# Kernel tuning notes

Measured on AMD Instinct MI355X. Metric: run time of the kernel, lower is better.

The kernel has to match this reference:

```python
import jax, jax.numpy as jnp
import numpy as np
import math

B, T, C = 4, 1024, 768
H, K = 12, 10
D = C // H  # 64


def setup_inputs() -> dict:
    key = jax.random.key(0)
    ks = jax.random.split(key, 8)
    s = 1.0 / math.sqrt(C)
    return {
        "hidden_states": jax.random.normal(ks[0], (B, T, C), jnp.float32),
        "ucb_count_score": jax.random.uniform(ks[1], (B, H, T, T), jnp.float32),
        "Wq": jax.random.normal(ks[2], (C, C), jnp.float32) * s,
        "bq": jnp.zeros((C,), jnp.float32),
        "Wk": jax.random.normal(ks[3], (C, C), jnp.float32) * s,
        "bk": jnp.zeros((C,), jnp.float32),
        "Wv": jax.random.normal(ks[4], (C, C), jnp.float32) * s,
        "bv": jnp.zeros((C,), jnp.float32),
        "Wo": jax.random.normal(ks[5], (C, C), jnp.float32) * s,
        "bo": jnp.zeros((C,), jnp.float32),
        "counter": 2000,
        "ucb": 1,
    }


def _heads(x):
    # [B,T,C] -> [B,H,T,D]
    return x.reshape(B, T, H, D).transpose(0, 2, 1, 3)


def reference(hidden_states, ucb_count_score, Wq, bq, Wk, bk, Wv, bv, Wo, bo, counter, ucb):
    q = _heads(hidden_states @ Wq + bq)
    k = _heads(hidden_states @ Wk + bk)
    v = _heads(hidden_states @ Wv + bv)

    scores = jnp.einsum("bhqd,bhkd->bhqk", q, k) / math.sqrt(D)
    att = jax.nn.softmax(scores, axis=-1)

    if ucb and counter >= 1000:  # ucb_activation_step
        log_t = math.log(float(counter))
        ucb_scores = att + 1.0 * jnp.sqrt(log_t / (ucb_count_score + 1e-8))  # ucb_beta=1.0
        _, top_idx = jax.lax.top_k(ucb_scores, K)  # [B,H,T,K]
        # scatter 1.0 at top-k positions along last axis
        flat_idx = top_idx.reshape(-1, K)            # [N,K], N=B*H*T
        n = flat_idx.shape[0]
        mask = jnp.zeros((n, T), att.dtype).at[jnp.arange(n)[:, None], flat_idx].set(1.0)
        mask = mask.reshape(B, H, T, T)
        updated_count = ucb_count_score + mask
        sel = att * mask
        attention_probs = sel / (sel.sum(axis=-1, keepdims=True) + 1e-8)
    else:
        attention_probs = att
        updated_count = ucb_count_score

    ctx = jnp.einsum("bhqk,bhkd->bhqd", attention_probs, v)
    ctx = ctx.transpose(0, 2, 1, 3).reshape(B, T, C)
    out = ctx @ Wo + bo  # proj_dropout is identity in eval
    return out, attention_probs, updated_count
```

## Files before the change

### kernel.cpp

```cpp
#include <hip/hip_runtime.h>
#include <math.h>

namespace {

constexpr int Bc = 4, Tc = 1024, Cch = 768, Hc = 12, Dc = 64, KSEL = 10;
constexpr size_t BTC    = (size_t)Bc * Tc * Cch;
constexpr size_t PROBSN = (size_t)Bc * Hc * Tc * Tc;
constexpr size_t CC     = (size_t)Cch * Cch;

typedef __attribute__((ext_vector_type(8))) short          bf16x8;
typedef __attribute__((ext_vector_type(4))) float          f32x4;
typedef __attribute__((ext_vector_type(4))) unsigned short u16x4;
typedef __attribute__((ext_vector_type(8))) unsigned short u16x8;

__device__ __forceinline__ unsigned short bf16rne(float x) {
  unsigned int u = __float_as_uint(x);
  return (unsigned short)((u + 0x7FFFu + ((u >> 16) & 1u)) >> 16);
}
__device__ __forceinline__ float bf16tof(unsigned short h) {
  return __uint_as_float(((unsigned int)h) << 16);
}

__global__ __launch_bounds__(256) void split_plane(
    const float* __restrict__ src,
    unsigned short* __restrict__ h, unsigned short* __restrict__ l)
{
  const size_t i = (size_t)(blockIdx.x * 256 + threadIdx.x) * 4;
  const float4 v = *(const float4*)&src[i];
  const float xs[4] = {v.x, v.y, v.z, v.w};
  u16x4 hh, ll;
  #pragma unroll
  for (int e = 0; e < 4; ++e) {
    const unsigned short hb = bf16rne(xs[e]);
    hh[e] = hb;
    ll[e] = bf16rne(xs[e] - bf16tof(hb));
  }
  *(u16x4*)&h[i] = hh;
  *(u16x4*)&l[i] = ll;
}

__global__ __launch_bounds__(256) void splitT_w(
    const float* __restrict__ W,
    unsigned short* __restrict__ th, unsigned short* __restrict__ tl)
{
  __shared__ float tile[32][33];
  const int n0 = blockIdx.x * 32, k0 = blockIdx.y * 32;
  const int x = threadIdx.x & 31, y = threadIdx.x >> 5;

  #pragma unroll
  for (int i = 0; i < 4; ++i) {
    const int kk = y * 4 + i;
    tile[kk][x] = W[(size_t)(k0 + kk) * Cch + n0 + x];
  }
  __syncthreads();
  #pragma unroll
  for (int i = 0; i < 4; ++i) {
    const int nn = y * 4 + i;
    const float v = tile[x][nn];
    const unsigned short hb = bf16rne(v);
    th[(size_t)(n0 + nn) * Cch + k0 + x] = hb;
    tl[(size_t)(n0 + nn) * Cch + k0 + x] = bf16rne(v - bf16tof(hb));
  }
}

__global__ __launch_bounds__(256) void qkv_mfma(
    const unsigned short* __restrict__ hidh, const unsigned short* __restrict__ hidl,
    const unsigned short* __restrict__ wqth, const unsigned short* __restrict__ wqtl,
    const unsigned short* __restrict__ wkth, const unsigned short* __restrict__ wktl,
    const unsigned short* __restrict__ wvth, const unsigned short* __restrict__ wvtl,
    const float* __restrict__ bq, const float* __restrict__ bk,
    const float* __restrict__ bv,
    unsigned short* __restrict__ qh, unsigned short* __restrict__ ql,
    unsigned short* __restrict__ kh, unsigned short* __restrict__ kl,
    float* __restrict__ V)
{
  const int z = blockIdx.z;
  const unsigned short* __restrict__ Bhp = (z == 0) ? wqth : (z == 1) ? wkth : wvth;
  const unsigned short* __restrict__ Blp = (z == 0) ? wqtl : (z == 1) ? wktl : wvtl;
  const float* __restrict__ bias = (z == 0) ? bq : (z == 1) ? bk : bv;

  const int m0 = blockIdx.y * 64;
  const int n0 = blockIdx.x * 128;

  __shared__ unsigned short Ah[64][72],  Al[64][72];
  __shared__ unsigned short Bh[128][72], Bl[128][72];

  const int t    = threadIdx.x;
  const int lane = t & 63;
  const int wv   = t >> 6;
  const int wq   = (wv >> 1) * 32;
  const int wk   = (wv & 1) * 64;
  const int fr   = lane & 15;
  const int fg   = lane >> 4;

  f32x4 acc[2][4] = {};

  for (int k0 = 0; k0 < Cch; k0 += 64) {
    __syncthreads();
    #pragma unroll
    for (int i = 0; i < 2; ++i) {
      const int id = t + 256*i;
      const int r = id >> 3, c8 = (id & 7) * 8;
      *(u16x8*)&Ah[r][c8] = *(const u16x8*)&hidh[(size_t)(m0 + r)*Cch + k0 + c8];
      *(u16x8*)&Al[r][c8] = *(const u16x8*)&hidl[(size_t)(m0 + r)*Cch + k0 + c8];
    }
    #pragma unroll
    for (int i = 0; i < 4; ++i) {
      const int id = t + 256*i;
      const int r = id >> 3, c8 = (id & 7) * 8;
      *(u16x8*)&Bh[r][c8] = *(const u16x8*)&Bhp[(size_t)(n0 + r)*Cch + k0 + c8];
      *(u16x8*)&Bl[r][c8] = *(const u16x8*)&Blp[(size_t)(n0 + r)*Cch + k0 + c8];
    }
    __syncthreads();

    #pragma unroll
    for (int g2 = 0; g2 < 2; ++g2) {
      const int dof = g2*32 + 8*fg;
      bf16x8 aH[2], aL[2];
      #pragma unroll
      for (int qt = 0; qt < 2; ++qt) {
        aH[qt] = *(const bf16x8*)&Ah[wq + qt*16 + fr][dof];
        aL[qt] = *(const bf16x8*)&Al[wq + qt*16 + fr][dof];
      }
      #pragma unroll
      for (int kt = 0; kt < 4; ++kt) {
        const bf16x8 bH = *(const bf16x8*)&Bh[wk + kt*16 + fr][dof];
        const bf16x8 bL = *(const bf16x8*)&Bl[wk + kt*16 + fr][dof];
        #pragma unroll
        for (int qt = 0; qt < 2; ++qt) {
          acc[qt][kt] = __builtin_amdgcn_mfma_f32_16x16x32_bf16(
              aH[qt], bH, acc[qt][kt], 0, 0, 0);
          acc[qt][kt] = __builtin_amdgcn_mfma_f32_16x16x32_bf16(
              aH[qt], bL, acc[qt][kt], 0, 0, 0);
          acc[qt][kt] = __builtin_amdgcn_mfma_f32_16x16x32_bf16(
              aL[qt], bH, acc[qt][kt], 0, 0, 0);
        }
      }
    }
  }

  float bcol[4];
  #pragma unroll
  for (int kt = 0; kt < 4; ++kt) bcol[kt] = bias[n0 + wk + kt*16 + fr];

  unsigned short* __restrict__ dh = (z == 0) ? qh : kh;
  unsigned short* __restrict__ dl = (z == 0) ? ql : kl;

  #pragma unroll
  for (int qt = 0; qt < 2; ++qt) {
    #pragma unroll
    for (int j = 0; j < 4; ++j) {
      const int m  = m0 + wq + qt*16 + 4*fg + j;
      const int b  = m >> 10, tt = m & 1023;
      #pragma unroll
      for (int kt = 0; kt < 4; ++kt) {
        const int col = n0 + wk + kt*16 + fr;
        const float val = acc[qt][kt][j] + bcol[kt];
        const size_t idx =
            (((size_t)(b*Hc + (col >> 6)))*Tc + tt)*Dc + (col & 63);
        if (z < 2) {
          const unsigned short hb = bf16rne(val);
          dh[idx] = hb;
          dl[idx] = bf16rne(val - bf16tof(hb));
        } else {
          V[idx] = val;
        }
      }
    }
  }
}

__global__ __launch_bounds__(256) void score_mfma(
    const unsigned short* __restrict__ qhp, const unsigned short* __restrict__ qlp,
    const unsigned short* __restrict__ khp, const unsigned short* __restrict__ klp,
    float* __restrict__ scores)
{
  const int k0 = blockIdx.x * 128;
  const int q0 = blockIdx.y * 64;
  const int bh = blockIdx.z;

  __shared__ unsigned short Qh[64][72],  Ql[64][72];
  __shared__ unsigned short Kh[128][72], Kl[128][72];

  const int t = threadIdx.x;
  const size_t qb = ((size_t)bh*Tc + q0) * Dc;
  const size_t kb = ((size_t)bh*Tc + k0) * Dc;

  #pragma unroll
  for (int i = 0; i < 2; ++i) {
    const int id = t + 256*i;
    const int r = id >> 3, c8 = (id & 7) * 8;
    *(u16x8*)&Qh[r][c8] = *(const u16x8*)&qhp[qb + (size_t)r*Dc + c8];
    *(u16x8*)&Ql[r][c8] = *(const u16x8*)&qlp[qb + (size_t)r*Dc + c8];
  }
  #pragma unroll
  for (int i = 0; i < 4; ++i) {
    const int id = t + 256*i;
    const int r = id >> 3, c8 = (id & 7) * 8;
    *(u16x8*)&Kh[r][c8] = *(const u16x8*)&khp[kb + (size_t)r*Dc + c8];
    *(u16x8*)&Kl[r][c8] = *(const u16x8*)&klp[kb + (size_t)r*Dc + c8];
  }
  __syncthreads();

  const int lane = t & 63;
  const int wv   = t >> 6;
  const int wq   = (wv >> 1) * 32;
  const int wk   = (wv & 1) * 64;
  const int fr   = lane & 15;
  const int fg   = lane >> 4;

  f32x4 acc[2][4] = {};

  #pragma unroll
  for (int g2 = 0; g2 < 2; ++g2) {
    const int dof = g2*32 + 8*fg;
    bf16x8 aH[2], aL[2];
    #pragma unroll
    for (int qt = 0; qt < 2; ++qt) {
      aH[qt] = *(const bf16x8*)&Qh[wq + qt*16 + fr][dof];
      aL[qt] = *(const bf16x8*)&Ql[wq + qt*16 + fr][dof];
    }
    #pragma unroll
    for (int kt = 0; kt < 4; ++kt) {
      const bf16x8 bH = *(const bf16x8*)&Kh[wk + kt*16 + fr][dof];
      const bf16x8 bL = *(const bf16x8*)&Kl[wk + kt*16 + fr][dof];
      #pragma unroll
      for (int qt = 0; qt < 2; ++qt) {
        acc[qt][kt] = __builtin_amdgcn_mfma_f32_16x16x32_bf16(
            aH[qt], bH, acc[qt][kt], 0, 0, 0);
        acc[qt][kt] = __builtin_amdgcn_mfma_f32_16x16x32_bf16(
            aH[qt], bL, acc[qt][kt], 0, 0, 0);
        acc[qt][kt] = __builtin_amdgcn_mfma_f32_16x16x32_bf16(
            aL[qt], bH, acc[qt][kt], 0, 0, 0);
      }
    }
  }

  #pragma unroll
  for (int qt = 0; qt < 2; ++qt) {
    #pragma unroll
    for (int j = 0; j < 4; ++j) {
      const int qrow = q0 + wq + qt*16 + 4*fg + j;
      const size_t rb = ((size_t)bh * Tc + qrow) * Tc + k0 + wk;
      #pragma unroll
      for (int kt = 0; kt < 4; ++kt)
        scores[rb + kt*16 + fr] = acc[qt][kt][j] * 0.125f;
    }
  }
}

__global__ __launch_bounds__(256, 4) void ucb_topk(
    const float* __restrict__ qkv,
    const float* __restrict__ count_in,
    const int*   __restrict__ counter_p,
    const int*   __restrict__ ucb_p,
    float* __restrict__ probs,
    float* __restrict__ count_out,
    float* __restrict__ ctx)
{
  const int bh   = blockIdx.y;
  const int lane = threadIdx.x & 63;
  const int wv   = threadIdx.x >> 6;
  const int row  = blockIdx.x * 4 + wv;
  const int b = bh / Hc, h = bh % Hc;
  const size_t rb = ((size_t)bh * Tc + row) * Tc;
  const float* __restrict__ Vh = qkv + 2*BTC + (size_t)bh * Tc * Dc;

  __shared__ float psel[4][KSEL];

  const int  counter = counter_p[0];
  const int  ucbf    = ucb_p[0];
  const bool do_ucb  = (ucbf != 0) && (counter >= 1000);
  const float lt     = do_ucb ? logf((float)counter) : 0.f;

  float s[16];
  #pragma unroll
  for (int w = 0; w < 16; ++w) s[w] = probs[rb + lane + 64*w];

  float mx = -INFINITY;
  #pragma unroll
  for (int w = 0; w < 16; ++w) mx = fmaxf(mx, s[w]);
  #pragma unroll
  for (int off = 32; off > 0; off >>= 1) mx = fmaxf(mx, __shfl_xor(mx, off));

  float sum = 0.f;
  #pragma unroll
  for (int w = 0; w < 16; ++w) { s[w] = __expf(s[w] - mx); sum += s[w]; }
  #pragma unroll
  for (int off = 32; off > 0; off >>= 1) sum += __shfl_xor(sum, off);

  const float rsum = 1.0f / sum;
  #pragma unroll
  for (int w = 0; w < 16; ++w) s[w] = s[w] * rsum;

  if (do_ucb) {
    const float sqlt = sqrtf(lt);

    unsigned long long key[16];
    #pragma unroll
    for (int w = 0; w < 16; ++w) {
      const float c = count_in[rb + lane + 64*w];
      count_out[rb + lane + 64*w] = c;
      const float u = fmaf(sqlt, rsqrtf(c + 1e-8f), s[w]);
      key[w] = ((unsigned long long)__float_as_uint(u) << 32)
             | (unsigned long long)(~(unsigned)(lane + (w << 6)));
    }

    unsigned selmask = 0u;
    unsigned long long rpack = 0ull;
    int ks[KSEL];

    #pragma unroll
    for (int r = 0; r < KSEL; ++r) {
      unsigned long long m = 0ull;
      #pragma unroll
      for (int w = 0; w < 16; ++w) {
        const unsigned long long kw =
            ((selmask >> w) & 1u) ? 0ull : key[w];
        m = (kw > m) ? kw : m;
      }
      #pragma unroll
      for (int off = 32; off > 0; off >>= 1) {
        const unsigned long long o = __shfl_xor(m, off);
        m = (o > m) ? o : m;
      }
      const int idx = (int)(~(unsigned)(m & 0xFFFFFFFFull));
      ks[r] = __builtin_amdgcn_readfirstlane(idx);
      if ((idx & 63) == lane) {
        const int wsel = idx >> 6;
        selmask |= (1u << wsel);
        rpack   |= ((unsigned long long)r << (wsel * 4));
      }
    }

    #pragma unroll
    for (int w = 0; w < 16; ++w) {
      if ((selmask >> w) & 1u) {
        const int r = (int)((rpack >> (4 * w)) & 15ull);
        psel[wv][r] = s[w];
      }
    }
    __syncthreads();

    float pvv[KSEL];
    float denom = 1e-8f;
    #pragma unroll
    for (int r = 0; r < KSEL; ++r) { pvv[r] = psel[wv][r]; denom += pvv[r]; }
    const float rden = 1.0f / denom;

    #pragma unroll
    for (int w = 0; w < 16; ++w) {
      const bool sb = (selmask >> w) & 1u;
      probs[rb + lane + 64*w] = sb ? (s[w] * rden) : 0.0f;
    }
    #pragma unroll
    for (int r = 0; r < KSEL; ++r) {
      if ((ks[r] & 63) == lane)
        count_out[rb + ks[r]] = count_in[rb + ks[r]] + 1.0f;
    }

    float cd = 0.f;
    #pragma unroll
    for (int r = 0; r < KSEL; ++r)
      cd += pvv[r] * Vh[(size_t)ks[r] * Dc + lane];
    ctx[((size_t)b*Tc + row)*Cch + h*Dc + lane] = cd * rden;
  } else {
    #pragma unroll
    for (int w = 0; w < 16; ++w) {
      probs[rb + lane + 64*w]     = s[w];
      count_out[rb + lane + 64*w] = count_in[rb + lane + 64*w];
    }
  }
}

__global__ __launch_bounds__(256) void pv_gemm(
    const float* __restrict__ probs,
    const float* __restrict__ Vm,
    float* __restrict__ ctx,
    const int* __restrict__ counter_p,
    const int* __restrict__ ucb_p)
{
  if ((ucb_p[0] != 0) && (counter_p[0] >= 1000)) return;

  const int bh = blockIdx.y;
  const int q0 = blockIdx.x * 64;
  const int b = bh / Hc, h = bh % Hc;

  __shared__ float aT[32][68];
  __shared__ float vN[32][68];

  const int t  = threadIdx.x;
  const int tn = t & 15;
  const int tq = t >> 4;

  float acc[4][4];
  #pragma unroll
  for (int i = 0; i < 4; ++i)
    #pragma unroll
    for (int j = 0; j < 4; ++j) acc[i][j] = 0.f;

  for (int k0 = 0; k0 < Tc; k0 += 32) {
    __syncthreads();
    #pragma unroll
    for (int p = 0; p < 2; ++p) {
      const int id = t + 256*p;
      const int r = id >> 3, c = id & 7;
      const float4 v =
          *(const float4*)&probs[((size_t)bh*Tc + q0 + r)*Tc + k0 + 4*c];
      aT[4*c + 0][r] = v.x; aT[4*c + 1][r] = v.y;
      aT[4*c + 2][r] = v.z; aT[4*c + 3][r] = v.w;
    }
    #pragma unroll
    for (int p = 0; p < 2; ++p) {
      const int id = t + 256*p;
      const int kk = id >> 4, dcc = id & 15;
      const float4 v = *(const float4*)&Vm[((size_t)bh*Tc + k0 + kk)*Dc + 4*dcc];
      *(float4*)&vN[kk][4*dcc] = v;
    }
    __syncthreads();
    #pragma unroll
    for (int kk = 0; kk < 32; ++kk) {
      const float4 a  = *(const float4*)&aT[kk][4*tq];
      const float4 vv = *(const float4*)&vN[kk][4*tn];
      const float av[4] = {a.x, a.y, a.z, a.w};
      const float bw[4] = {vv.x, vv.y, vv.z, vv.w};
      #pragma unroll
      for (int qi = 0; qi < 4; ++qi)
        #pragma unroll
        for (int ni = 0; ni < 4; ++ni) acc[qi][ni] += av[qi] * bw[ni];
    }
  }

  #pragma unroll
  for (int qi = 0; qi < 4; ++qi) {
    const int tt = q0 + 4*tq + qi;
    float4 o;
    o.x = acc[qi][0]; o.y = acc[qi][1]; o.z = acc[qi][2]; o.w = acc[qi][3];
    *(float4*)&ctx[((size_t)b*Tc + tt)*Cch + h*Dc + 4*tn] = o;
  }
}

__global__ __launch_bounds__(256) void out_mfma(
    const unsigned short* __restrict__ ah, const unsigned short* __restrict__ al,
    const unsigned short* __restrict__ bth, const unsigned short* __restrict__ btl,
    const float* __restrict__ bias,
    float* __restrict__ out)
{
  const int m0 = blockIdx.y * 64;
  const int n0 = blockIdx.x * 128;

  __shared__ unsigned short Ah[64][72],  Al[64][72];
  __shared__ unsigned short Bh[128][72], Bl[128][72];

  const int t    = threadIdx.x;
  const int lane = t & 63;
  const int wv   = t >> 6;
  const int wq   = (wv >> 1) * 32;
  const int wk   = (wv & 1) * 64;
  const int fr   = lane & 15;
  const int fg   = lane >> 4;

  f32x4 acc[2][4] = {};

  for (int k0 = 0; k0 < Cch; k0 += 64) {
    __syncthreads();
    #pragma unroll
    for (int i = 0; i < 2; ++i) {
      const int id = t + 256*i;
      const int r = id >> 3, c8 = (id & 7) * 8;
      *(u16x8*)&Ah[r][c8] = *(const u16x8*)&ah[(size_t)(m0 + r)*Cch + k0 + c8];
      *(u16x8*)&Al[r][c8] = *(const u16x8*)&al[(size_t)(m0 + r)*Cch + k0 + c8];
    }
    #pragma unroll
    for (int i = 0; i < 4; ++i) {
      const int id = t + 256*i;
      const int r = id >> 3, c8 = (id & 7) * 8;
      *(u16x8*)&Bh[r][c8] = *(const u16x8*)&bth[(size_t)(n0 + r)*Cch + k0 + c8];
      *(u16x8*)&Bl[r][c8] = *(const u16x8*)&btl[(size_t)(n0 + r)*Cch + k0 + c8];
    }
    __syncthreads();

    #pragma unroll
    for (int g2 = 0; g2 < 2; ++g2) {
      const int dof = g2*32 + 8*fg;
      bf16x8 aH[2], aL[2];
      #pragma unroll
      for (int qt = 0; qt < 2; ++qt) {
        aH[qt] = *(const bf16x8*)&Ah[wq + qt*16 + fr][dof];
        aL[qt] = *(const bf16x8*)&Al[wq + qt*16 + fr][dof];
      }
      #pragma unroll
      for (int kt = 0; kt < 4; ++kt) {
        const bf16x8 bH = *(const bf16x8*)&Bh[wk + kt*16 + fr][dof];
        const bf16x8 bL = *(const bf16x8*)&Bl[wk + kt*16 + fr][dof];
        #pragma unroll
        for (int qt = 0; qt < 2; ++qt) {
          acc[qt][kt] = __builtin_amdgcn_mfma_f32_16x16x32_bf16(
              aH[qt], bH, acc[qt][kt], 0, 0, 0);
          acc[qt][kt] = __builtin_amdgcn_mfma_f32_16x16x32_bf16(
              aH[qt], bL, acc[qt][kt], 0, 0, 0);
          acc[qt][kt] = __builtin_amdgcn_mfma_f32_16x16x32_bf16(
              aL[qt], bH, acc[qt][kt], 0, 0, 0);
        }
      }
    }
  }

  float bcol[4];
  #pragma unroll
  for (int kt = 0; kt < 4; ++kt) bcol[kt] = bias[n0 + wk + kt*16 + fr];

  #pragma unroll
  for (int qt = 0; qt < 2; ++qt) {
    #pragma unroll
    for (int j = 0; j < 4; ++j) {
      const int m = m0 + wq + qt*16 + 4*fg + j;
      #pragma unroll
      for (int kt = 0; kt < 4; ++kt) {
        const int col = n0 + wk + kt*16 + fr;
        out[(size_t)m * Cch + col] = acc[qt][kt][j] + bcol[kt];
      }
    }
  }
}

}

extern "C" void kernel_launch(void* const* d_in, const int* in_sizes, int n_in,
                              void* d_out, int out_size, void* d_ws, size_t ws_size,
                              hipStream_t stream) {
  (void)in_sizes; (void)n_in; (void)out_size; (void)ws_size;

  const float* hid  = (const float*)d_in[0];
  const float* cnt  = (const float*)d_in[1];
  const float* Wq   = (const float*)d_in[2];
  const float* bq   = (const float*)d_in[3];
  const float* Wk   = (const float*)d_in[4];
  const float* bk   = (const float*)d_in[5];
  const float* Wv   = (const float*)d_in[6];
  const float* bv   = (const float*)d_in[7];
  const float* Wo   = (const float*)d_in[8];
  const float* bo   = (const float*)d_in[9];
  const int* counter = (const int*)d_in[10];
  const int* ucb     = (const int*)d_in[11];

  float* out       = (float*)d_out;
  float* probs     = out + BTC;
  float* count_out = probs + PROBSN;

  float* ws  = (float*)d_ws;
  float* V   = ws + 2*BTC;
  float* ctx = ws + 3*BTC;
  unsigned short* qkb = (unsigned short*)d_ws;
  unsigned short* qh = qkb;
  unsigned short* ql = qkb + BTC;
  unsigned short* kh = qkb + 2*BTC;
  unsigned short* kl = qkb + 3*BTC;

  unsigned short* cvt  = (unsigned short*)count_out;
  unsigned short* hidh = cvt;
  unsigned short* hidl = cvt + BTC;
  unsigned short* wqth = cvt + 2*BTC;
  unsigned short* wqtl = wqth + CC;
  unsigned short* wkth = wqtl + CC;
  unsigned short* wktl = wkth + CC;
  unsigned short* wvth = wktl + CC;
  unsigned short* wvtl = wvth + CC;

  unsigned short* ctxh = qkb;
  unsigned short* ctxl = qkb + BTC;
  unsigned short* woth = qkb + 2*BTC;
  unsigned short* wotl = woth + CC;

  split_plane<<<BTC/1024, 256, 0, stream>>>(hid, hidh, hidl);
  splitT_w<<<dim3(24, 24), 256, 0, stream>>>(Wq, wqth, wqtl);
  splitT_w<<<dim3(24, 24), 256, 0, stream>>>(Wk, wkth, wktl);
  splitT_w<<<dim3(24, 24), 256, 0, stream>>>(Wv, wvth, wvtl);

  qkv_mfma<<<dim3(Cch/128, (Bc*Tc)/64, 3), 256, 0, stream>>>(
      hidh, hidl, wqth, wqtl, wkth, wktl, wvth, wvtl,
      bq, bk, bv, qh, ql, kh, kl, V);

  score_mfma<<<dim3(Tc/128, Tc/64, Bc*Hc), 256, 0, stream>>>(
      qh, ql, kh, kl, probs);

  ucb_topk<<<dim3(Tc/4, Bc*Hc), 256, 0, stream>>>(
      ws, cnt, counter, ucb, probs, count_out, ctx);

  pv_gemm<<<dim3(Tc/64, Bc*Hc), 256, 0, stream>>>(
      probs, V, ctx, counter, ucb);

  split_plane<<<BTC/1024, 256, 0, stream>>>(ctx, ctxh, ctxl);
  splitT_w<<<dim3(24, 24), 256, 0, stream>>>(Wo, woth, wotl);

  out_mfma<<<dim3(Cch/128, (Bc*Tc)/64), 256, 0, stream>>>(
      ctxh, ctxl, woth, wotl, bo, out);
}
```

Before: 390.0 us.

## Fuse QK^T score computation into softmax/UCB top-k kernel

Merges the score GEMM kernel into the softmax/top-k kernel. Each 1024-thread block now computes scores for 16 query rows against all keys in 128-key chunks through shared memory, so the full fp32 score matrix no longer makes a write-then-read round trip through global memory. The cost is reloading K tiles for every 16-row block instead of every 64-row block. It also adds three syncthreads per chunk and uses a large 1024-thread block whose occupancy may be limited by register and LDS pressure.

Result: slower. 495.4 us (+27.0%).

```diff
diff --git a/kernel.cpp b/kernel.cpp
--- a/kernel.cpp
+++ b/kernel.cpp
@@ -170,86 +170,9 @@
   }
 }
 
-__global__ __launch_bounds__(256) void score_mfma(
+__global__ __launch_bounds__(1024, 4) void score_topk(
     const unsigned short* __restrict__ qhp, const unsigned short* __restrict__ qlp,
     const unsigned short* __restrict__ khp, const unsigned short* __restrict__ klp,
-    float* __restrict__ scores)
-{
-  const int k0 = blockIdx.x * 128;
-  const int q0 = blockIdx.y * 64;
-  const int bh = blockIdx.z;
-
-  __shared__ unsigned short Qh[64][72],  Ql[64][72];
-  __shared__ unsigned short Kh[128][72], Kl[128][72];
-
-  const int t = threadIdx.x;
-  const size_t qb = ((size_t)bh*Tc + q0) * Dc;
-  const size_t kb = ((size_t)bh*Tc + k0) * Dc;
-
-  #pragma unroll
-  for (int i = 0; i < 2; ++i) {
-    const int id = t + 256*i;
-    const int r = id >> 3, c8 = (id & 7) * 8;
-    *(u16x8*)&Qh[r][c8] = *(const u16x8*)&qhp[qb + (size_t)r*Dc + c8];
-    *(u16x8*)&Ql[r][c8] = *(const u16x8*)&qlp[qb + (size_t)r*Dc + c8];
-  }
-  #pragma unroll
-  for (int i = 0; i < 4; ++i) {
-    const int id = t + 256*i;
-    const int r = id >> 3, c8 = (id & 7) * 8;
-    *(u16x8*)&Kh[r][c8] = *(const u16x8*)&khp[kb + (size_t)r*Dc + c8];
-    *(u16x8*)&Kl[r][c8] = *(const u16x8*)&klp[kb + (size_t)r*Dc + c8];
-  }
-  __syncthreads();
-
-  const int lane = t & 63;
-  const int wv   = t >> 6;
-  const int wq   = (wv >> 1) * 32;
-  const int wk   = (wv & 1) * 64;
-  const int fr   = lane & 15;
-  const int fg   = lane >> 4;
-
-  f32x4 acc[2][4] = {};
-
-  #pragma unroll
-  for (int g2 = 0; g2 < 2; ++g2) {
-    const int dof = g2*32 + 8*fg;
-    bf16x8 aH[2], aL[2];
-    #pragma unroll
-    for (int qt = 0; qt < 2; ++qt) {
-      aH[qt] = *(const bf16x8*)&Qh[wq + qt*16 + fr][dof];
-      aL[qt] = *(const bf16x8*)&Ql[wq + qt*16 + fr][dof];
-    }
-    #pragma unroll
-    for (int kt = 0; kt < 4; ++kt) {
-      const bf16x8 bH = *(const bf16x8*)&Kh[wk + kt*16 + fr][dof];
-      const bf16x8 bL = *(const bf16x8*)&Kl[wk + kt*16 + fr][dof];
-      #pragma unroll
-      for (int qt = 0; qt < 2; ++qt) {
-        acc[qt][kt] = __builtin_amdgcn_mfma_f32_16x16x32_bf16(
-            aH[qt], bH, acc[qt][kt], 0, 0, 0);
-        acc[qt][kt] = __builtin_amdgcn_mfma_f32_16x16x32_bf16(
-            aH[qt], bL, acc[qt][kt], 0, 0, 0);
-        acc[qt][kt] = __builtin_amdgcn_mfma_f32_16x16x32_bf16(
-            aL[qt], bH, acc[qt][kt], 0, 0, 0);
-      }
-    }
-  }
-
-  #pragma unroll
-  for (int qt = 0; qt < 2; ++qt) {
-    #pragma unroll
-    for (int j = 0; j < 4; ++j) {
-      const int qrow = q0 + wq + qt*16 + 4*fg + j;
-      const size_t rb = ((size_t)bh * Tc + qrow) * Tc + k0 + wk;
-      #pragma unroll
-      for (int kt = 0; kt < 4; ++kt)
-        scores[rb + kt*16 + fr] = acc[qt][kt][j] * 0.125f;
-    }
-  }
-}
-
-__global__ __launch_bounds__(256, 4) void ucb_topk(
     const float* __restrict__ qkv,
     const float* __restrict__ count_in,
     const int*   __restrict__ counter_p,
@@ -258,24 +181,82 @@
     float* __restrict__ count_out,
     float* __restrict__ ctx)
 {
-  const int bh   = blockIdx.y;
-  const int lane = threadIdx.x & 63;
-  const int wv   = threadIdx.x >> 6;
-  const int row  = blockIdx.x * 4 + wv;
-  const int b = bh / Hc, h = bh % Hc;
+  const int bh = blockIdx.y;
+  const int q0 = blockIdx.x * 16;
+  const int b  = bh / Hc, h = bh % Hc;
+
+  __shared__ unsigned short Qh[16][72],  Ql[16][72];
+  __shared__ unsigned short Kh[128][72], Kl[128][72];
+  __shared__ float scA[16][136], scB[16][136];
+  __shared__ float psel[16][KSEL];
+
+  const int t    = threadIdx.x;
+  const int lane = t & 63;
+  const int wv   = t >> 6;
+  const int fr   = lane & 15;
+  const int fg   = lane >> 4;
+  const int half = wv >> 3;
+  const int c0   = (wv & 7) * 16;
+
+  {
+    const size_t qb = ((size_t)bh*Tc + q0) * Dc;
+    if (t < 128) {
+      const int r = t >> 3, c8 = (t & 7) * 8;
+      *(u16x8*)&Qh[r][c8] = *(const u16x8*)&qhp[qb + (size_t)r*Dc + c8];
+    } else if (t < 256) {
+      const int t2 = t - 128;
+      const int r = t2 >> 3, c8 = (t2 & 7) * 8;
+      *(u16x8*)&Ql[r][c8] = *(const u16x8*)&qlp[qb + (size_t)r*Dc + c8];
+    }
+  }
+
+  const int krr = t >> 3, kc8 = (t & 7) * 8;
+
+  float s[16];
+  #pragma unroll
+  for (int j = 0; j < 8; ++j) {
+    __syncthreads();
+    {
+      const size_t kb = ((size_t)bh*Tc + j*128) * Dc;
+      *(u16x8*)&Kh[krr][kc8] = *(const u16x8*)&khp[kb + (size_t)krr*Dc + kc8];
+      *(u16x8*)&Kl[krr][kc8] = *(const u16x8*)&klp[kb + (size_t)krr*Dc + kc8];
+    }
+    __syncthreads();
+    f32x4 acc = {};
+    #pragma unroll
+    for (int g2 = 0; g2 < 2; ++g2) {
+      const int dof = g2*32 + 8*fg;
+      const bf16x8 bH = *(const bf16x8*)&Kh[c0 + fr][dof];
+      if (half == 0) {
+        const bf16x8 aH = *(const bf16x8*)&Qh[fr][dof];
+        const bf16x8 bL = *(const bf16x8*)&Kl[c0 + fr][dof];
+        acc = __builtin_amdgcn_mfma_f32_16x16x32_bf16(aH, bH, acc, 0, 0, 0);
+        acc = __builtin_amdgcn_mfma_f32_16x16x32_bf16(aH, bL, acc, 0, 0, 0);
+      } else {
+        const bf16x8 aL = *(const bf16x8*)&Ql[fr][dof];
+        acc = __builtin_amdgcn_mfma_f32_16x16x32_bf16(aL, bH, acc, 0, 0, 0);
+      }
+    }
+    if (half == 0) {
+      #pragma unroll
+      for (int e = 0; e < 4; ++e) scA[4*fg + e][c0 + fr] = acc[e];
+    } else {
+      #pragma unroll
+      for (int e = 0; e < 4; ++e) scB[4*fg + e][c0 + fr] = acc[e];
+    }
+    __syncthreads();
+    s[2*j]     = (scA[wv][lane]      + scB[wv][lane])      * 0.125f;
+    s[2*j + 1] = (scA[wv][64 + lane] + scB[wv][64 + lane]) * 0.125f;
+  }
+
+  const int row = q0 + wv;
   const size_t rb = ((size_t)bh * Tc + row) * Tc;
   const float* __restrict__ Vh = qkv + 2*BTC + (size_t)bh * Tc * Dc;
-
-  __shared__ float psel[4][KSEL];
 
   const int  counter = counter_p[0];
   const int  ucbf    = ucb_p[0];
   const bool do_ucb  = (ucbf != 0) && (counter >= 1000);
   const float lt     = do_ucb ? logf((float)counter) : 0.f;
-
-  float s[16];
-  #pragma unroll
-  for (int w = 0; w < 16; ++w) s[w] = probs[rb + lane + 64*w];
 
   float mx = -INFINITY;
   #pragma unroll
@@ -581,11 +562,8 @@
       hidh, hidl, wqth, wqtl, wkth, wktl, wvth, wvtl,
       bq, bk, bv, qh, ql, kh, kl, V);
 
-  score_mfma<<<dim3(Tc/128, Tc/64, Bc*Hc), 256, 0, stream>>>(
-      qh, ql, kh, kl, probs);
-
-  ucb_topk<<<dim3(Tc/4, Bc*Hc), 256, 0, stream>>>(
-      ws, cnt, counter, ucb, probs, count_out, ctx);
+  score_topk<<<dim3(Tc/16, Bc*Hc), 1024, 0, stream>>>(
+      qh, ql, kh, kl, ws, cnt, counter, ucb, probs, count_out, ctx);
 
   pv_gemm<<<dim3(Tc/64, Bc*Hc), 256, 0, stream>>>(
       probs, V, ctx, counter, ucb);
```

## Process two rows per wave in UCB top-k and use float argmax keys

Applied to the files above, without the earlier changes.

Each wavefront in the softmax and top-k kernel now handles two attention rows at once, interleaving their loads, reductions and selection rounds to raise instruction-level parallelism and memory requests in flight. The 64-bit packed key max is replaced by a float value plus an int index, with the lowest index winning ties in the cross-lane reduction. Launch bounds drop to 2 blocks per CU and the grid is halved, so register pressure and occupancy trade against the extra per-wave work.

New measurement: 414.5 us. 6.3% more time.

```diff
diff --git a/kernel.cpp b/kernel.cpp
--- a/kernel.cpp
+++ b/kernel.cpp
@@ -249,7 +249,7 @@
   }
 }
 
-__global__ __launch_bounds__(256, 4) void ucb_topk(
+__global__ __launch_bounds__(256, 2) void ucb_topk(
     const float* __restrict__ qkv,
     const float* __restrict__ count_in,
     const int*   __restrict__ counter_p,
@@ -261,114 +261,149 @@
   const int bh   = blockIdx.y;
   const int lane = threadIdx.x & 63;
   const int wv   = threadIdx.x >> 6;
-  const int row  = blockIdx.x * 4 + wv;
+  const int rowA = blockIdx.x * 8 + wv * 2;
+  const int rowB = rowA + 1;
   const int b = bh / Hc, h = bh % Hc;
-  const size_t rb = ((size_t)bh * Tc + row) * Tc;
+  const size_t rbA = ((size_t)bh * Tc + rowA) * Tc;
+  const size_t rbB = ((size_t)bh * Tc + rowB) * Tc;
   const float* __restrict__ Vh = qkv + 2*BTC + (size_t)bh * Tc * Dc;
 
-  __shared__ float psel[4][KSEL];
+  __shared__ float psel[8][KSEL];
 
   const int  counter = counter_p[0];
   const int  ucbf    = ucb_p[0];
   const bool do_ucb  = (ucbf != 0) && (counter >= 1000);
   const float lt     = do_ucb ? logf((float)counter) : 0.f;
 
-  float s[16];
-  #pragma unroll
-  for (int w = 0; w < 16; ++w) s[w] = probs[rb + lane + 64*w];
-
-  float mx = -INFINITY;
-  #pragma unroll
-  for (int w = 0; w < 16; ++w) mx = fmaxf(mx, s[w]);
-  #pragma unroll
-  for (int off = 32; off > 0; off >>= 1) mx = fmaxf(mx, __shfl_xor(mx, off));
-
-  float sum = 0.f;
-  #pragma unroll
-  for (int w = 0; w < 16; ++w) { s[w] = __expf(s[w] - mx); sum += s[w]; }
-  #pragma unroll
-  for (int off = 32; off > 0; off >>= 1) sum += __shfl_xor(sum, off);
-
-  const float rsum = 1.0f / sum;
-  #pragma unroll
-  for (int w = 0; w < 16; ++w) s[w] = s[w] * rsum;
+  float sA[16], sB[16];
+  #pragma unroll
+  for (int w = 0; w < 16; ++w) sA[w] = probs[rbA + lane + 64*w];
+  #pragma unroll
+  for (int w = 0; w < 16; ++w) sB[w] = probs[rbB + lane + 64*w];
+
+  float mxA = -INFINITY, mxB = -INFINITY;
+  #pragma unroll
+  for (int w = 0; w < 16; ++w) { mxA = fmaxf(mxA, sA[w]); mxB = fmaxf(mxB, sB[w]); }
+  #pragma unroll
+  for (int off = 32; off > 0; off >>= 1) {
+    mxA = fmaxf(mxA, __shfl_xor(mxA, off));
+    mxB = fmaxf(mxB, __shfl_xor(mxB, off));
+  }
+  float smA = 0.f, smB = 0.f;
+  #pragma unroll
+  for (int w = 0; w < 16; ++w) {
+    sA[w] = __expf(sA[w] - mxA); smA += sA[w];
+    sB[w] = __expf(sB[w] - mxB); smB += sB[w];
+  }
+  #pragma unroll
+  for (int off = 32; off > 0; off >>= 1) {
+    smA += __shfl_xor(smA, off);
+    smB += __shfl_xor(smB, off);
+  }
+  const float rsA = 1.0f / smA, rsB = 1.0f / smB;
+  #pragma unroll
+  for (int w = 0; w < 16; ++w) { sA[w] *= rsA; sB[w] *= rsB; }
 
   if (do_ucb) {
     const float sqlt = sqrtf(lt);
 
-    unsigned long long key[16];
+    float uA[16], uB[16];
     #pragma unroll
     for (int w = 0; w < 16; ++w) {
-      const float c = count_in[rb + lane + 64*w];
-      count_out[rb + lane + 64*w] = c;
-      const float u = fmaf(sqlt, rsqrtf(c + 1e-8f), s[w]);
-      key[w] = ((unsigned long long)__float_as_uint(u) << 32)
-             | (unsigned long long)(~(unsigned)(lane + (w << 6)));
-    }
-
-    unsigned selmask = 0u;
-    unsigned long long rpack = 0ull;
-    int ks[KSEL];
+      const float cA = count_in[rbA + lane + 64*w];
+      count_out[rbA + lane + 64*w] = cA;
+      uA[w] = fmaf(sqlt, rsqrtf(cA + 1e-8f), sA[w]);
+      const float cB = count_in[rbB + lane + 64*w];
+      count_out[rbB + lane + 64*w] = cB;
+      uB[w] = fmaf(sqlt, rsqrtf(cB + 1e-8f), sB[w]);
+    }
+
+    unsigned selA = 0u, selB = 0u;
+    unsigned long long rpA = 0ull, rpB = 0ull;
+    int ksA[KSEL], ksB[KSEL];
 
     #pragma unroll
     for (int r = 0; r < KSEL; ++r) {
-      unsigned long long m = 0ull;
-      #pragma unroll
-      for (int w = 0; w < 16; ++w) {
-        const unsigned long long kw =
-            ((selmask >> w) & 1u) ? 0ull : key[w];
-        m = (kw > m) ? kw : m;
-      }
+      float bvA = ((selA >> 0) & 1u) ? -INFINITY : uA[0];  int bwA = 0;
+      float bvB = ((selB >> 0) & 1u) ? -INFINITY : uB[0];  int bwB = 0;
+      #pragma unroll
+      for (int w = 1; w < 16; ++w) {
+        const float tA = ((selA >> w) & 1u) ? -INFINITY : uA[w];
+        if (tA > bvA) { bvA = tA; bwA = w; }
+        const float tB = ((selB >> w) & 1u) ? -INFINITY : uB[w];
+        if (tB > bvB) { bvB = tB; bwB = w; }
+      }
+      int kA = lane + (bwA << 6);
+      int kB = lane + (bwB << 6);
       #pragma unroll
       for (int off = 32; off > 0; off >>= 1) {
-        const unsigned long long o = __shfl_xor(m, off);
-        m = (o > m) ? o : m;
-      }
-      const int idx = (int)(~(unsigned)(m & 0xFFFFFFFFull));
-      ks[r] = __builtin_amdgcn_readfirstlane(idx);
-      if ((idx & 63) == lane) {
-        const int wsel = idx >> 6;
-        selmask |= (1u << wsel);
-        rpack   |= ((unsigned long long)r << (wsel * 4));
+        const float ovA = __shfl_xor(bvA, off);
+        const int   okA = __shfl_xor(kA,  off);
+        const float ovB = __shfl_xor(bvB, off);
+        const int   okB = __shfl_xor(kB,  off);
+        if (ovA > bvA || (ovA == bvA && okA < kA)) { bvA = ovA; kA = okA; }
+        if (ovB > bvB || (ovB == bvB && okB < kB)) { bvB = ovB; kB = okB; }
+      }
+      ksA[r] = __builtin_amdgcn_readfirstlane(kA);
+      ksB[r] = __builtin_amdgcn_readfirstlane(kB);
+      if ((kA & 63) == lane) {
+        const int wsel = kA >> 6;
+        selA |= 1u << wsel;
+        rpA  |= ((unsigned long long)r) << (4 * wsel);
+      }
+      if ((kB & 63) == lane) {
+        const int wsel = kB >> 6;
+        selB |= 1u << wsel;
+        rpB  |= ((unsigned long long)r) << (4 * wsel);
       }
     }
 
     #pragma unroll
     for (int w = 0; w < 16; ++w) {
-      if ((selmask >> w) & 1u) {
-        const int r = (int)((rpack >> (4 * w)) & 15ull);
-        psel[wv][r] = s[w];
-      }
+      if ((selA >> w) & 1u)
+        psel[2*wv    ][(int)((rpA >> (4 * w)) & 15ull)] = sA[w];
+      if ((selB >> w) & 1u)
+        psel[2*wv + 1][(int)((rpB >> (4 * w)) & 15ull)] = sB[w];
     }
     __syncthreads();
 
-    float pvv[KSEL];
-    float denom = 1e-8f;
-    #pragma unroll
-    for (int r = 0; r < KSEL; ++r) { pvv[r] = psel[wv][r]; denom += pvv[r]; }
-    const float rden = 1.0f / denom;
+    float pvvA[KSEL], pvvB[KSEL];
+    float denA = 1e-8f, denB = 1e-8f;
+    #pragma unroll
+    for (int r = 0; r < KSEL; ++r) {
+      pvvA[r] = psel[2*wv][r];     denA += pvvA[r];
+      pvvB[r] = psel[2*wv + 1][r]; denB += pvvB[r];
+    }
+    const float rdA = 1.0f / denA, rdB = 1.0f / denB;
 
     #pragma unroll
     for (int w = 0; w < 16; ++w) {
-      const bool sb = (selmask >> w) & 1u;
-      probs[rb + lane + 64*w] = sb ? (s[w] * rden) : 0.0f;
+      probs[rbA + lane + 64*w] = ((selA >> w) & 1u) ? (sA[w] * rdA) : 0.0f;
+      probs[rbB + lane + 64*w] = ((selB >> w) & 1u) ? (sB[w] * rdB) : 0.0f;
     }
     #pragma unroll
     for (int r = 0; r < KSEL; ++r) {
-      if ((ks[r] & 63) == lane)
-        count_out[rb + ks[r]] = count_in[rb + ks[r]] + 1.0f;
-    }
-
-    float cd = 0.f;
-    #pragma unroll
-    for (int r = 0; r < KSEL; ++r)
-      cd += pvv[r] * Vh[(size_t)ks[r] * Dc + lane];
-    ctx[((size_t)b*Tc + row)*Cch + h*Dc + lane] = cd * rden;
+      if ((ksA[r] & 63) == lane)
+        count_out[rbA + ksA[r]] = count_in[rbA + ksA[r]] + 1.0f;
+      if ((ksB[r] & 63) == lane)
+        count_out[rbB + ksB[r]] = count_in[rbB + ksB[r]] + 1.0f;
+    }
+
+    float cdA = 0.f, cdB = 0.f;
+    #pragma unroll
+    for (int r = 0; r < KSEL; ++r) {
+      cdA += pvvA[r] * Vh[(size_t)ksA[r] * Dc + lane];
+      cdB += pvvB[r] * Vh[(size_t)ksB[r] * Dc + lane];
+    }
+    ctx[((size_t)b*Tc + rowA)*Cch + h*Dc + lane] = cdA * rdA;
+    ctx[((size_t)b*Tc + rowB)*Cch + h*Dc + lane] = cdB * rdB;
   } else {
     #pragma unroll
     for (int w = 0; w < 16; ++w) {
-      probs[rb + lane + 64*w]     = s[w];
-      count_out[rb + lane + 64*w] = count_in[rb + lane + 64*w];
+      probs[rbA + lane + 64*w]     = sA[w];
+      count_out[rbA + lane + 64*w] = count_in[rbA + lane + 64*w];
+      probs[rbB + lane + 64*w]     = sB[w];
+      count_out[rbB + lane + 64*w] = count_in[rbB + lane + 64*w];
     }
   }
 }
@@ -584,7 +619,7 @@
   score_mfma<<<dim3(Tc/128, Tc/64, Bc*Hc), 256, 0, stream>>>(
       qh, ql, kh, kl, probs);
 
-  ucb_topk<<<dim3(Tc/4, Bc*Hc), 256, 0, stream>>>(
+  ucb_topk<<<dim3(Tc/8, Bc*Hc), 256, 0, stream>>>(
       ws, cnt, counter, ucb, probs, count_out, ctx);
 
   pv_gemm<<<dim3(Tc/64, Bc*Hc), 256, 0, stream>>>(
```
